# Kernel tuning notes

Measured on AMD Instinct MI355X. Metric: run time of the kernel, lower is better.

## Reference

```python
import jax, jax.numpy as jnp
import numpy as np

N_NODES = 50000
N_EDGES = 1600000
IN_DIM = 512
OUT_DIM = 256


def setup_inputs() -> dict:
    key = jax.random.key(0)
    k1, k2, k3, k4, k5, k6 = jax.random.split(key, 6)
    inputs = jax.random.normal(k1, (N_NODES, IN_DIM), dtype=jnp.float32)
    edge_row = jax.random.randint(k2, (N_EDGES,), 0, N_NODES, dtype=jnp.int32)
    edge_col = jax.random.randint(k3, (N_EDGES,), 0, N_NODES, dtype=jnp.int32)
    edge_val = jax.random.uniform(k4, (N_EDGES,), dtype=jnp.float32)
    stdv = 1.0 / np.sqrt(OUT_DIM)
    weight = jax.random.uniform(k5, (IN_DIM, OUT_DIM), dtype=jnp.float32, minval=-stdv, maxval=stdv)
    bias = jax.random.uniform(k6, (OUT_DIM,), dtype=jnp.float32, minval=-stdv, maxval=stdv)
    return {"inputs": inputs, "edge_row": edge_row, "edge_col": edge_col,
            "edge_val": edge_val, "weight": weight, "bias": bias}


def reference(inputs, edge_row, edge_col, edge_val, weight, bias):
    # dense GEMM: [N, in] @ [in, out] -> [N, out]
    support = inputs @ weight
    # SpMM: out[r] += val * support[c] for each edge (r, c, val)
    gathered = edge_val[:, None] * support[edge_col]  # [E, out]
    output = jax.ops.segment_sum(gathered, edge_row, num_segments=N_NODES)
    return output + bias
```

## Files before the change

### kernel.cpp

```cpp
#include <hip/hip_runtime.h>

#define N_NODES 50000
#define N_EDGES 1600000
#define IN_DIM 512
#define OUT_DIM 256

#define BM 64
#define BN 256
#define BK 32
#define APAD 8
#define LDA (BK + APAD)

#define RPB   128
#define NBKT  391
#define CHUNK 4096
#define CAP   5120

typedef unsigned int u32;
typedef unsigned short u16;
typedef short bf16x8 __attribute__((ext_vector_type(8)));
typedef float f32x4 __attribute__((ext_vector_type(4)));

__device__ __forceinline__ float bf_to_f(u16 u) { return __uint_as_float(((u32)u) << 16); }
__device__ __forceinline__ u16 f_to_bf(float f) {
    u32 u = __float_as_uint(f);
    u32 r = (u + 0x7fffu + ((u >> 16) & 1u)) >> 16;
    return (u16)r;
}

__global__ __launch_bounds__(256) void zero_cur(int* __restrict__ cursor) {
    const int i = blockIdx.x * 256 + threadIdx.x;
    if (i < NBKT) cursor[i] = 0;
}

__global__ __launch_bounds__(256) void scatter1(const int* __restrict__ er,
                                                const int* __restrict__ ec,
                                                const float* __restrict__ ev,
                                                int* __restrict__ cursor,
                                                int2* __restrict__ tmp) {
    __shared__ int  hcnt[NBKT];
    __shared__ int  loff[NBKT];
    __shared__ int  gbase[NBKT];
    __shared__ int  sc[512];
    __shared__ int2 estage[CHUNK];
    __shared__ u16  bslot[CHUNK];

    const int t = threadIdx.x;
    const int base = blockIdx.x * CHUNK;
    const int nedge = min(CHUNK, N_EDGES - base);

    for (int k = t; k < NBKT; k += 256) hcnt[k] = 0;
    __syncthreads();

    int w0[16], w1[16], rk[16];
    #pragma unroll
    for (int j = 0; j < 16; ++j) {
        const int i = j * 256 + t;
        rk[j] = -1;
        if (i < nedge) {
            const int e = base + i;
            const int r = er[e];
            const int bk = r >> 7;
            w0[j] = ec[e] | ((r & 127) << 16) | (bk << 23);
            w1[j] = __float_as_int(ev[e]);
            rk[j] = atomicAdd(&hcnt[bk], 1);
        }
    }
    __syncthreads();

    sc[t]       = (t < NBKT) ? hcnt[t] : 0;
    sc[t + 256] = (t + 256 < NBKT) ? hcnt[t + 256] : 0;
    __syncthreads();
    #pragma unroll
    for (int off = 1; off < 512; off <<= 1) {
        const int a0 = (t >= off) ? sc[t - off] : 0;
        const int a1 = sc[t + 256 - off];
        __syncthreads();
        sc[t] += a0;
        sc[t + 256] += a1;
        __syncthreads();
    }
    if (t < NBKT)       loff[t]       = sc[t] - hcnt[t];
    if (t + 256 < NBKT) loff[t + 256] = sc[t + 256] - hcnt[t + 256];

    if (t < NBKT && hcnt[t] > 0)
        gbase[t] = t * CAP + atomicAdd(&cursor[t], hcnt[t]);
    if (t + 256 < NBKT && hcnt[t + 256] > 0)
        gbase[t + 256] = (t + 256) * CAP + atomicAdd(&cursor[t + 256], hcnt[t + 256]);
    __syncthreads();

    #pragma unroll
    for (int j = 0; j < 16; ++j) {
        if (rk[j] >= 0) {
            const int bk = ((u32)w0[j]) >> 23;
            const int s = loff[bk] + rk[j];
            estage[s] = make_int2(w0[j], w1[j]);
            bslot[s]  = (u16)bk;
        }
    }
    __syncthreads();

    for (int s = t; s < nedge; s += 256) {
        const int bk = bslot[s];
        const int2 e2 = estage[s];
        const int gpos = gbase[bk] + (s - loff[bk]);
        if (gpos < (bk + 1) * CAP)
            tmp[gpos] = e2;
    }
}

__global__ __launch_bounds__(256) void scatter2(const int* __restrict__ cursor,
                                                const int2* __restrict__ tmp,
                                                int* __restrict__ row_ptr,
                                                int2* __restrict__ sedge) {
    __shared__ int sc[512];
    __shared__ int orig[512];
    __shared__ int rcnt[RPB];
    __shared__ int rsc[RPB];
    __shared__ int rcur[RPB];
    const int t = threadIdx.x;
    const int b = blockIdx.x;

    const int c0 = (t < NBKT) ? min(cursor[t], CAP) : 0;
    const int c1 = (t + 256 < NBKT) ? min(cursor[t + 256], CAP) : 0;
    sc[t] = c0;       orig[t] = c0;
    sc[t + 256] = c1; orig[t + 256] = c1;
    __syncthreads();
    #pragma unroll
    for (int off = 1; off < 512; off <<= 1) {
        const int a0 = (t >= off) ? sc[t - off] : 0;
        const int a1 = sc[t + 256 - off];
        __syncthreads();
        sc[t] += a0;
        sc[t + 256] += a1;
        __syncthreads();
    }
    const int gb = sc[b] - orig[b];
    const int n  = orig[b];
    const int2* src = tmp + (size_t)b * CAP;

    if (b == 0 && t == 0) row_ptr[N_NODES] = N_EDGES;

    if (t < RPB) rcnt[t] = 0;
    __syncthreads();
    for (int i = t; i < n; i += 256)
        atomicAdd(&rcnt[(((u32)src[i].x) >> 16) & 127], 1);
    __syncthreads();

    if (t < RPB) rsc[t] = rcnt[t];
    __syncthreads();
    #pragma unroll
    for (int off = 1; off < RPB; off <<= 1) {
        int a = 0;
        if (t < RPB && t >= off) a = rsc[t - off];
        __syncthreads();
        if (t < RPB) rsc[t] += a;
        __syncthreads();
    }
    if (t < RPB) {
        const int excl = rsc[t] - rcnt[t];
        rcur[t] = gb + excl;
        const int row = b * RPB + t;
        if (row < N_NODES) row_ptr[row] = gb + excl;
    }
    __syncthreads();

    for (int i = t; i < n; i += 256) {
        const int2 e2 = src[i];
        const int rloc = (((u32)e2.x) >> 16) & 127;
        const int pos = atomicAdd(&rcur[rloc], 1);
        sedge[pos] = make_int2(e2.x & 0xFFFF, e2.y);
    }
}

__global__ __launch_bounds__(256) void wcvt(const float* __restrict__ W,
                                            u16* __restrict__ WT) {
    const int n  = threadIdx.x;
    const int k0 = blockIdx.x * 4;
    ushort4 o;
    o.x = f_to_bf(W[(size_t)(k0 + 0) * OUT_DIM + n]);
    o.y = f_to_bf(W[(size_t)(k0 + 1) * OUT_DIM + n]);
    o.z = f_to_bf(W[(size_t)(k0 + 2) * OUT_DIM + n]);
    o.w = f_to_bf(W[(size_t)(k0 + 3) * OUT_DIM + n]);
    *(ushort4*)(WT + (size_t)n * IN_DIM + k0) = o;
}

__global__ __launch_bounds__(256) void gemm_mfma(const float* __restrict__ X,
                                                 const u16* __restrict__ WT,
                                                 u16* __restrict__ Sb) {
    __shared__ u16 As[BM * LDA];
    __shared__ u16 Bs[BN * LDA];

    const int tid  = threadIdx.x;
    const int wave = tid >> 6;
    const int lane = tid & 63;
    const int r0   = blockIdx.x * BM;
    const int wn   = wave * 64;
    const int l15  = lane & 15;
    const int quad = lane >> 4;

    f32x4 acc[4][4];
    #pragma unroll
    for (int i = 0; i < 4; ++i)
        #pragma unroll
        for (int j = 0; j < 4; ++j) acc[i][j] = (f32x4)0.f;

    const int arow = tid >> 2;
    const int akp  = (tid & 3) * 8;
    const int xrow = min(r0 + arow, N_NODES - 1);
    const float* xsrc = X + (size_t)xrow * IN_DIM + akp;
    const int brow = tid >> 1;
    const int bkp  = (tid & 1) * 16;
    const u16* bsrc = WT + (size_t)brow * IN_DIM + bkp;

    for (int kc = 0; kc < IN_DIM; kc += BK) {
        {
            const float4 f0 = *(const float4*)(xsrc + kc + 0);
            const float4 f1 = *(const float4*)(xsrc + kc + 4);
            ushort4 p0, p1;
            p0.x = f_to_bf(f0.x); p0.y = f_to_bf(f0.y); p0.z = f_to_bf(f0.z); p0.w = f_to_bf(f0.w);
            p1.x = f_to_bf(f1.x); p1.y = f_to_bf(f1.y); p1.z = f_to_bf(f1.z); p1.w = f_to_bf(f1.w);
            *(ushort4*)&As[arow * LDA + akp + 0] = p0;
            *(ushort4*)&As[arow * LDA + akp + 4] = p1;
        }
        {
            const uint4 b0 = *(const uint4*)(bsrc + kc);
            const uint4 b1 = *(const uint4*)(bsrc + kc + 8);
            *(uint4*)&Bs[brow * LDA + bkp + 0] = b0;
            *(uint4*)&Bs[brow * LDA + bkp + 8] = b1;
            const u16* bsrc2 = bsrc + (size_t)128 * IN_DIM;
            const uint4 b2 = *(const uint4*)(bsrc2 + kc);
            const uint4 b3 = *(const uint4*)(bsrc2 + kc + 8);
            *(uint4*)&Bs[(brow + 128) * LDA + bkp + 0] = b2;
            *(uint4*)&Bs[(brow + 128) * LDA + bkp + 8] = b3;
        }
        __syncthreads();

        bf16x8 af[4], bfr[4];
        #pragma unroll
        for (int mt = 0; mt < 4; ++mt)
            af[mt] = *(const bf16x8*)&As[(mt * 16 + l15) * LDA + quad * 8];
        #pragma unroll
        for (int nt = 0; nt < 4; ++nt)
            bfr[nt] = *(const bf16x8*)&Bs[(wn + nt * 16 + l15) * LDA + quad * 8];
        #pragma unroll
        for (int mt = 0; mt < 4; ++mt)
            #pragma unroll
            for (int nt = 0; nt < 4; ++nt)
                acc[mt][nt] = __builtin_amdgcn_mfma_f32_16x16x32_bf16(
                    af[mt], bfr[nt], acc[mt][nt], 0, 0, 0);
        __syncthreads();
    }

    #pragma unroll
    for (int mt = 0; mt < 4; ++mt) {
        #pragma unroll
        for (int r = 0; r < 4; ++r) {
            const int grow = r0 + mt * 16 + quad * 4 + r;
            if (grow < N_NODES) {
                u16* dst = Sb + (size_t)grow * OUT_DIM + wn + l15;
                #pragma unroll
                for (int nt = 0; nt < 4; ++nt)
                    dst[nt * 16] = f_to_bf(acc[mt][nt][r]);
            }
        }
    }
}

__global__ __launch_bounds__(256) void csr_spmm(const int* __restrict__ row_ptr,
                                                const int2* __restrict__ sedge,
                                                const u16* __restrict__ Sb,
                                                const float* __restrict__ bias,
                                                float* __restrict__ out) {
    const int wave = threadIdx.x >> 6;
    const int lane = threadIdx.x & 63;
    const int r = blockIdx.x * 4 + wave;
    if (r >= N_NODES) return;

    const int start = row_ptr[r];
    const int end   = row_ptr[r + 1];

    float4 acc = *(const float4*)(bias + lane * 4);
    const u16* sbase = Sb + lane * 4;

    for (int e = start; e < end; e += 8) {
        int2 ed[8];
        #pragma unroll
        for (int j = 0; j < 8; ++j) {
            const int idx = min(e + j, end - 1);
            ed[j] = sedge[idx];
        }
        #pragma unroll
        for (int j = 0; j < 8; ++j)
            if (e + j >= end) ed[j].y = 0;

        ushort4 sv[8];
        #pragma unroll
        for (int j = 0; j < 8; ++j)
            sv[j] = *(const ushort4*)(sbase + (size_t)ed[j].x * OUT_DIM);

        #pragma unroll
        for (int j = 0; j < 8; ++j) {
            const float vj = __int_as_float(ed[j].y);
            acc.x += vj * bf_to_f(sv[j].x);
            acc.y += vj * bf_to_f(sv[j].y);
            acc.z += vj * bf_to_f(sv[j].z);
            acc.w += vj * bf_to_f(sv[j].w);
        }
    }

    *(float4*)(out + (size_t)r * OUT_DIM + lane * 4) = acc;
}

extern "C" void kernel_launch(void* const* d_in, const int* in_sizes, int n_in,
                              void* d_out, int out_size, void* d_ws, size_t ws_size,
                              hipStream_t stream) {
    const float* X    = (const float*)d_in[0];
    const int*   er   = (const int*)d_in[1];
    const int*   ec   = (const int*)d_in[2];
    const float* ev   = (const float*)d_in[3];
    const float* W    = (const float*)d_in[4];
    const float* bias = (const float*)d_in[5];
    float* out        = (float*)d_out;

    char* ws = (char*)d_ws;
    u16*  Sb      = (u16*) (ws);
    int2* tmp     = (int2*)(ws);
    int*  cursor  = (int*) (ws + 16100000);
    int2* sedge   = (int2*)(ws + 25600000);
    u16*  WT      = (u16*) (ws + 38400000);
    int*  row_ptr = (int*) (ws + 38662144);

    hipLaunchKernelGGL(zero_cur, dim3(2), dim3(256), 0, stream, cursor);
    hipLaunchKernelGGL(scatter1, dim3((N_EDGES + CHUNK - 1) / CHUNK), dim3(256), 0,
                       stream, er, ec, ev, cursor, tmp);
    hipLaunchKernelGGL(scatter2, dim3(NBKT), dim3(256), 0, stream,
                       cursor, tmp, row_ptr, sedge);
    hipLaunchKernelGGL(wcvt, dim3(IN_DIM / 4), dim3(256), 0, stream, W, WT);
    hipLaunchKernelGGL(gemm_mfma, dim3((N_NODES + BM - 1) / BM), dim3(256), 0,
                       stream, X, WT, Sb);
    hipLaunchKernelGGL(csr_spmm, dim3((N_NODES + 3) / 4), dim3(256), 0, stream,
                       row_ptr, sedge, Sb, bias, out);
}
```

Baseline: 358.9 us.

## Store GEMM output column-chunked and split SpMM across eight column chunks

The GEMM now writes the bf16 support matrix in a chunked layout of 8 slabs, each holding 32 columns per node. The SpMM launches 8 blocks per row group, one per column chunk, so each slab (about 3.2 MB) can stay cache-resident while rows are gathered. Within a wave, 8 edge slots work in parallel and their partial sums are combined with xor shuffles. The cost is that every chunk block rereads the edge list (8x more edge reads), and each gather is only 64 bytes per row, so memory accesses become more scattered.

```diff
diff --git a/kernel.cpp b/kernel.cpp
--- a/kernel.cpp
+++ b/kernel.cpp
@@ -187,7 +187,7 @@
 
 __global__ __launch_bounds__(256) void gemm_mfma(const float* __restrict__ X,
                                                  const u16* __restrict__ WT,
-                                                 u16* __restrict__ Sb) {
+                                                 u16* __restrict__ Sbc) {
     __shared__ u16 As[BM * LDA];
     __shared__ u16 Bs[BN * LDA];
 
@@ -258,58 +258,74 @@
         for (int r = 0; r < 4; ++r) {
             const int grow = r0 + mt * 16 + quad * 4 + r;
             if (grow < N_NODES) {
-                u16* dst = Sb + (size_t)grow * OUT_DIM + wn + l15;
                 #pragma unroll
-                for (int nt = 0; nt < 4; ++nt)
-                    dst[nt * 16] = f_to_bf(acc[mt][nt][r]);
+                for (int nt = 0; nt < 4; ++nt) {
+                    const int col = wn + nt * 16 + l15;
+                    Sbc[((size_t)(col >> 5) * N_NODES + grow) * 32 + (col & 31)]
+                        = f_to_bf(acc[mt][nt][r]);
+                }
             }
         }
     }
 }
 
-__global__ __launch_bounds__(256) void csr_spmm(const int* __restrict__ row_ptr,
-                                                const int2* __restrict__ sedge,
-                                                const u16* __restrict__ Sb,
-                                                const float* __restrict__ bias,
-                                                float* __restrict__ out) {
-    const int wave = threadIdx.x >> 6;
-    const int lane = threadIdx.x & 63;
-    const int r = blockIdx.x * 4 + wave;
-    if (r >= N_NODES) return;
+__global__ __launch_bounds__(256) void spmm_c8(const int* __restrict__ row_ptr,
+                                               const int2* __restrict__ sedge,
+                                               const u16* __restrict__ Sbc,
+                                               const float* __restrict__ bias,
+                                               float* __restrict__ out) {
+    const int bid   = blockIdx.x;
+    const int chunk = bid & 7;
+    const int rg    = bid >> 3;
+    const int wave  = threadIdx.x >> 6;
+    const int lane  = threadIdx.x & 63;
+    const int slot  = lane >> 3;
+    const int sub   = lane & 7;
+    const int r     = rg * 4 + wave;
 
     const int start = row_ptr[r];
     const int end   = row_ptr[r + 1];
 
-    float4 acc = *(const float4*)(bias + lane * 4);
-    const u16* sbase = Sb + lane * 4;
-
-    for (int e = start; e < end; e += 8) {
-        int2 ed[8];
-        #pragma unroll
-        for (int j = 0; j < 8; ++j) {
-            const int idx = min(e + j, end - 1);
-            ed[j] = sedge[idx];
-        }
-        #pragma unroll
-        for (int j = 0; j < 8; ++j)
-            if (e + j >= end) ed[j].y = 0;
-
-        ushort4 sv[8];
-        #pragma unroll
-        for (int j = 0; j < 8; ++j)
-            sv[j] = *(const ushort4*)(sbase + (size_t)ed[j].x * OUT_DIM);
-
-        #pragma unroll
-        for (int j = 0; j < 8; ++j) {
-            const float vj = __int_as_float(ed[j].y);
-            acc.x += vj * bf_to_f(sv[j].x);
-            acc.y += vj * bf_to_f(sv[j].y);
-            acc.z += vj * bf_to_f(sv[j].z);
-            acc.w += vj * bf_to_f(sv[j].w);
-        }
-    }
-
-    *(float4*)(out + (size_t)r * OUT_DIM + lane * 4) = acc;
+    const u16* sb = Sbc + (size_t)chunk * ((size_t)N_NODES * 32) + sub * 4;
+    float4 acc = make_float4(0.f, 0.f, 0.f, 0.f);
+
+    for (int e = start; e < end; e += 32) {
+        int   cols[4];
+        float vals[4];
+        #pragma unroll
+        for (int u = 0; u < 4; ++u) {
+            const int idx = e + u * 8 + slot;
+            const int2 ed = sedge[min(idx, end - 1)];
+            cols[u] = ed.x;
+            vals[u] = (idx < end) ? __int_as_float(ed.y) : 0.f;
+        }
+        ushort4 sv[4];
+        #pragma unroll
+        for (int u = 0; u < 4; ++u)
+            sv[u] = *(const ushort4*)(sb + (size_t)cols[u] * 32);
+        #pragma unroll
+        for (int u = 0; u < 4; ++u) {
+            acc.x += vals[u] * bf_to_f(sv[u].x);
+            acc.y += vals[u] * bf_to_f(sv[u].y);
+            acc.z += vals[u] * bf_to_f(sv[u].z);
+            acc.w += vals[u] * bf_to_f(sv[u].w);
+        }
+    }
+
+    #pragma unroll
+    for (int m = 8; m <= 32; m <<= 1) {
+        acc.x += __shfl_xor(acc.x, m);
+        acc.y += __shfl_xor(acc.y, m);
+        acc.z += __shfl_xor(acc.z, m);
+        acc.w += __shfl_xor(acc.w, m);
+    }
+    if (slot == 0) {
+        const float4 b4 = *(const float4*)(bias + chunk * 32 + sub * 4);
+        float4 o;
+        o.x = acc.x + b4.x; o.y = acc.y + b4.y;
+        o.z = acc.z + b4.z; o.w = acc.w + b4.w;
+        *(float4*)(out + (size_t)r * OUT_DIM + chunk * 32 + sub * 4) = o;
+    }
 }
 
 extern "C" void kernel_launch(void* const* d_in, const int* in_sizes, int n_in,
@@ -324,7 +340,7 @@
     float* out        = (float*)d_out;
 
     char* ws = (char*)d_ws;
-    u16*  Sb      = (u16*) (ws);
+    u16*  Sbc     = (u16*) (ws);
     int2* tmp     = (int2*)(ws);
     int*  cursor  = (int*) (ws + 16100000);
     int2* sedge   = (int2*)(ws + 25600000);
@@ -338,7 +354,7 @@
                        cursor, tmp, row_ptr, sedge);
     hipLaunchKernelGGL(wcvt, dim3(IN_DIM / 4), dim3(256), 0, stream, W, WT);
     hipLaunchKernelGGL(gemm_mfma, dim3((N_NODES + BM - 1) / BM), dim3(256), 0,
-                       stream, X, WT, Sb);
-    hipLaunchKernelGGL(csr_spmm, dim3((N_NODES + 3) / 4), dim3(256), 0, stream,
-                       row_ptr, sedge, Sb, bias, out);
-}
+                       stream, X, WT, Sbc);
+    hipLaunchKernelGGL(spmm_c8, dim3(8 * (N_NODES / 4)), dim3(256), 0, stream,
+                       row_ptr, sedge, Sbc, bias, out);
+}
```

Result: slower. 411.3 us (+14.6%).
